# Kernel tuning notes

Measured on AMD Instinct MI355X. Metric: run time of the kernel, lower is better.

Reference implementation:

```python
import jax, jax.numpy as jnp
import numpy as np

B, L, W, H = 4, 4096, 2048, 8
BW = W // H  # block width


def setup_inputs() -> dict:
    key = jax.random.key(0)
    k = jax.random.split(key, 5)
    std = 1.0 / np.sqrt(BW)  # w_init_variance_scale=1.0
    # a_param init: uniform ring in [0.9,0.999] then inverse-softplus
    u = jax.random.uniform(k[4], (W,), minval=0.9**2 + 1e-8, maxval=0.999**2 + 1e-8)
    a_param = jnp.log(jnp.exp(-0.5 * jnp.log(u)) - 1.0)
    return {
        "x": jax.random.normal(k[0], (B, L, W), dtype=jnp.float32),
        "segment_pos": jnp.arange(L, dtype=jnp.int32),
        "prev_h": jnp.zeros((B, W), dtype=jnp.float32),
        "ig_w": std * jax.random.normal(k[1], (H, BW, BW), dtype=jnp.float32),
        "ig_b": jnp.zeros((H, BW), dtype=jnp.float32),
        "ag_w": std * jax.random.normal(k[2], (H, BW, BW), dtype=jnp.float32),
        "ag_b": jnp.zeros((H, BW), dtype=jnp.float32),
        "a_param": a_param,
    }


@jax.custom_vjp
def sqrt_bound(x):
    return jnp.sqrt(x)

def _sb_fwd(x):
    return jnp.sqrt(x), x

def _sb_bwd(x, g):
    _MAX_SQRT_GRADIENT = 1000.0
    return (g / jnp.sqrt(jnp.clip(4.0 * x, 1.0 / _MAX_SQRT_GRADIENT**2)),)

sqrt_bound.defvjp(_sb_fwd, _sb_bwd)


def block_diag_linear(x, w, b):
    # x: [b,l,(h*i)] -> [b,l,h,i]; w: [h,i,j]; b: [h,j]
    bsz, l, _ = x.shape
    xr = x.reshape(bsz, l, H, BW)
    y = jnp.einsum("blhi,hij->blhj", xr, w) + b
    return y.reshape(bsz, l, W)


def reference(x, segment_pos, prev_h, ig_w, ig_b, ag_w, ag_b, a_param):
    reset = (segment_pos == 0)[None, :, None]  # [1,l,1] bool
    gate_x = jax.nn.sigmoid(block_diag_linear(x, ig_w, ig_b))
    gate_a = jax.nn.sigmoid(block_diag_linear(x, ag_w, ag_b))
    log_a = -8.0 * gate_a * jax.nn.softplus(a_param)  # [b,l,w]
    a = jnp.exp(log_a)
    a_square = jnp.exp(2.0 * log_a)
    gated_x = x * gate_x
    multiplier = sqrt_bound(1.0 - a_square)
    multiplier = jnp.where(reset, 1.0, multiplier)
    normalized_x = gated_x * multiplier.astype(x.dtype)
    a = a * (~reset)  # zero recurrence weight at document boundaries

    # linear scan h_t = a_t * h_{t-1} + x_t, accumulate in float32
    def step(h, inp):
        a_t, x_t = inp
        h = a_t.astype(jnp.float32) * h + x_t.astype(jnp.float32)
        return h, h.astype(x.dtype)

    a_t = jnp.swapaxes(jnp.broadcast_to(a, x.shape), 0, 1)  # [l,b,w]
    x_t = jnp.swapaxes(normalized_x, 0, 1)  # [l,b,w]
    last_h, y = jax.lax.scan(step, prev_h, (a_t, x_t))
    y = jnp.swapaxes(y, 0, 1)  # [b,l,w]
    return y, last_h
```

## Files before the change

kernel.cpp:

```cpp
#include <hip/hip_runtime.h>
#include <hip/hip_bf16.h>
#include <cmath>

#define Bq   4
#define Lq   4096
#define Wq   2048
#define Hq   8
#define Mq   (Bq*Lq)
#define TCH  64
#define CCH  (Lq/TCH)

typedef __bf16 bf16;
typedef __attribute__((ext_vector_type(8))) __bf16 bf16x8;
typedef __attribute__((ext_vector_type(4))) float  f32x4;

#define WS_WT    0
#define WS_C     (2*8*256*256*2)
#define WS_PH    (4u<<20)
#define WS_AGG   (WS_PH + (size_t)Mq*Wq*4)
#define WS_CARRY (WS_AGG + (size_t)Bq*CCH*Wq*8)

union pkPH { unsigned u; bf16 v[2]; };

__global__ __launch_bounds__(256) void prep2(const float* __restrict__ ig_w,
                                             const float* __restrict__ ag_w,
                                             const float* __restrict__ a_param,
                                             bf16* __restrict__ wt, float* __restrict__ c_arr) {
    __shared__ float t[64*65];
    int bid = blockIdx.x;
    int kt = bid & 3, nt = (bid >> 2) & 3, h = (bid >> 4) & 7, g = bid >> 7;
    const float* src = g ? ag_w : ig_w;
    int rr = threadIdx.x >> 6, cc = threadIdx.x & 63;
#pragma unroll
    for (int p = 0; p < 16; p++) {
        int kl = p*4 + rr;
        t[kl*65 + cc] = src[h*65536 + (kt*64 + kl)*256 + nt*64 + cc];
    }
    if (bid < 8) {
        float ap = a_param[bid*256 + threadIdx.x];
        c_arr[bid*256 + threadIdx.x] = 8.0f * log1pf(__expf(ap));
    }
    __syncthreads();
#pragma unroll
    for (int p = 0; p < 16; p++) {
        int nl = p*4 + rr;
        wt[((size_t)((g*8 + h)*256) + nt*64 + nl)*256 + kt*64 + cc] = (bf16)t[cc*65 + nl];
    }
}

__global__ __launch_bounds__(256) void gates_scan(
    const float* __restrict__ x, const int* __restrict__ segpos,
    const bf16* __restrict__ wt, const float* __restrict__ igb,
    const float* __restrict__ agb, const float* __restrict__ c_arr,
    unsigned* __restrict__ PH, float2* __restrict__ agg)
{
    union SharedU {
        struct { bf16 As[64*72]; bf16 Wxs[64*72]; bf16 Was[64*72]; } st;
        struct { float A_s[64*65]; float G_s[64*65]; } ep;
    };
    __shared__ SharedU sh;
    __shared__ float segA[4*64], segH[4*64];
    __shared__ unsigned char rs[64];

    const int tid = threadIdx.x;
    const int bx  = blockIdx.x, by = blockIdx.y;
    const int b   = bx >> 6,    c  = bx & 63;
    const int m0  = bx * 64;
    const int h   = by >> 2,    nt = by & 3;
    const int n0  = nt * 64;
    const int wofs = h*256 + n0;

    const int lane = tid & 63, wid = tid >> 6;
    const int wm = wid >> 1, wn = wid & 1;
    const int l16 = lane & 15, quad = lane >> 4;

    if (tid < 64) rs[tid] = (segpos[(m0 + tid) & (Lq-1)] == 0) ? 1 : 0;

    f32x4 accx[2][2], acca[2][2];
#pragma unroll
    for (int i = 0; i < 2; i++)
#pragma unroll
        for (int j = 0; j < 2; j++) {
            accx[i][j] = (f32x4){0.f,0.f,0.f,0.f};
            acca[i][j] = (f32x4){0.f,0.f,0.f,0.f};
        }

    const bf16* wtx = wt + ((size_t)((0*Hq + h)*256 + n0))*256;
    const bf16* wta = wt + ((size_t)((1*Hq + h)*256 + n0))*256;

    for (int kk = 0; kk < 256; kk += 64) {
        __syncthreads();
#pragma unroll
        for (int p = 0; p < 2; p++) {
            int lin = p*2048 + tid*8;
            int r = lin >> 6, cc = lin & 63;
            const float* gp = x + (size_t)(m0 + r)*Wq + h*256 + kk + cc;
            float4 f0 = *(const float4*)gp;
            float4 f1 = *(const float4*)(gp + 4);
            bf16x8 v;
            v[0]=(bf16)f0.x; v[1]=(bf16)f0.y; v[2]=(bf16)f0.z; v[3]=(bf16)f0.w;
            v[4]=(bf16)f1.x; v[5]=(bf16)f1.y; v[6]=(bf16)f1.z; v[7]=(bf16)f1.w;
            *(bf16x8*)&sh.st.As[r*72 + cc] = v;
        }
#pragma unroll
        for (int p = 0; p < 2; p++) {
            int lin = p*2048 + tid*8;
            int r = lin >> 6, cc = lin & 63;
            *(bf16x8*)&sh.st.Wxs[r*72 + cc] = *(const bf16x8*)&wtx[(size_t)r*256 + kk + cc];
            *(bf16x8*)&sh.st.Was[r*72 + cc] = *(const bf16x8*)&wta[(size_t)r*256 + kk + cc];
        }
        __syncthreads();
#pragma unroll
        for (int ks = 0; ks < 2; ks++) {
            bf16x8 af[2], bxf[2], baf[2];
#pragma unroll
            for (int i = 0; i < 2; i++) {
                af[i]  = *(bf16x8*)&sh.st.As [(wm*32 + i*16 + l16)*72 + ks*32 + quad*8];
                bxf[i] = *(bf16x8*)&sh.st.Wxs[(wn*32 + i*16 + l16)*72 + ks*32 + quad*8];
                baf[i] = *(bf16x8*)&sh.st.Was[(wn*32 + i*16 + l16)*72 + ks*32 + quad*8];
            }
#pragma unroll
            for (int i = 0; i < 2; i++)
#pragma unroll
                for (int j = 0; j < 2; j++) {
                    accx[i][j] = __builtin_amdgcn_mfma_f32_16x16x32_bf16(af[i], bxf[j], accx[i][j], 0, 0, 0);
                    acca[i][j] = __builtin_amdgcn_mfma_f32_16x16x32_bf16(af[i], baf[j], acca[i][j], 0, 0, 0);
                }
        }
    }
    __syncthreads();

#pragma unroll
    for (int i = 0; i < 2; i++)
#pragma unroll
        for (int j = 0; j < 2; j++) {
            int col = wn*32 + j*16 + l16;
            int wf  = wofs + col;
            float bxv = igb[wf], bav = agb[wf], cc2 = c_arr[wf];
#pragma unroll
            for (int r = 0; r < 4; r++) {
                int row = wm*32 + i*16 + quad*4 + r;
                float zx = accx[i][j][r] + bxv;
                float za = acca[i][j][r] + bav;
                float gx = __builtin_amdgcn_rcpf(1.f + __expf(-zx));
                float ga = __builtin_amdgcn_rcpf(1.f + __expf(-za));
                float la = -ga * cc2;
                float a  = __expf(la);
                float mult = __builtin_amdgcn_sqrtf(fmaf(-a, a, 1.f));
                if (rs[row]) { a = 0.f; mult = 1.f; }
                sh.ep.A_s[row*65 + col] = a;
                sh.ep.G_s[row*65 + col] = gx * mult;
            }
        }
    __syncthreads();

    const int col2 = tid & 63, seg = tid >> 6;
    float Pl[16], hl[16];
    {
        float A = 1.f, hv = 0.f;
        const float* xp = x + (size_t)(m0 + seg*16)*Wq + wofs + col2;
#pragma unroll
        for (int r = 0; r < 16; r++) {
            int row = seg*16 + r;
            float a  = sh.ep.A_s[row*65 + col2];
            float xn = sh.ep.G_s[row*65 + col2] * xp[(size_t)r*Wq];
            hv = fmaf(a, hv, xn);
            A *= a;
            Pl[r] = A; hl[r] = hv;
        }
        segA[seg*64 + col2] = A;
        segH[seg*64 + col2] = hv;
    }
    __syncthreads();
    float Ap = 1.f, Hp = 0.f;
#pragma unroll
    for (int s = 0; s < 3; s++)
        if (s < seg) {
            Hp = fmaf(segA[s*64 + col2], Hp, segH[s*64 + col2]);
            Ap *= segA[s*64 + col2];
        }

    unsigned* php = PH + (size_t)(m0 + seg*16)*Wq + wofs + col2;
#pragma unroll
    for (int r = 0; r < 16; r++) {
        float Pf = Ap * Pl[r];
        float Hf = fmaf(Pl[r], Hp, hl[r]);
        pkPH pk; pk.v[0] = (bf16)Pf; pk.v[1] = (bf16)Hf;
        php[(size_t)r*Wq] = pk.u;
    }

    if (seg == 3) {
        float Ach = Ap * Pl[15];
        float Hch = fmaf(Pl[15], Hp, hl[15]);
        agg[(size_t)(b*CCH + c)*Wq + wofs + col2] = make_float2(Ach, Hch);
    }
}

__global__ __launch_bounds__(256) void chain_scan(
    const float2* __restrict__ agg, const float* __restrict__ prev_h,
    float* __restrict__ carry, float* __restrict__ last_h)
{
    int tid = blockIdx.x*256 + threadIdx.x;
    int w = tid & (Wq - 1), b = tid >> 11;
    float h = prev_h[tid];
    for (int c = 0; c < CCH; c++) {
        int idx = (b*CCH + c)*Wq + w;
        carry[idx] = h;
        float2 ah = agg[idx];
        h = fmaf(ah.x, h, ah.y);
    }
    last_h[tid] = h;
}

__global__ __launch_bounds__(256) void apply_carry(
    const unsigned* __restrict__ PH, const float* __restrict__ carry,
    float* __restrict__ y)
{
    size_t i4 = ((size_t)blockIdx.x*256 + threadIdx.x) * 4;
    uint4 p = *(const uint4*)(PH + i4);
    int w = (int)(i4 & (Wq - 1));
    int m = (int)(i4 >> 11);
    int b = m >> 12;
    int c = (m & (Lq - 1)) >> 6;
    float4 cr4 = *(const float4*)(carry + (size_t)(b*CCH + c)*Wq + w);
    float4 o;
    pkPH k;
    k.u = p.x; o.x = fmaf((float)k.v[0], cr4.x, (float)k.v[1]);
    k.u = p.y; o.y = fmaf((float)k.v[0], cr4.y, (float)k.v[1]);
    k.u = p.z; o.z = fmaf((float)k.v[0], cr4.z, (float)k.v[1]);
    k.u = p.w; o.w = fmaf((float)k.v[0], cr4.w, (float)k.v[1]);
    *(float4*)(y + i4) = o;
}

extern "C" void kernel_launch(void* const* d_in, const int* in_sizes, int n_in,
                              void* d_out, int out_size, void* d_ws, size_t ws_size,
                              hipStream_t stream) {
    const float* x       = (const float*)d_in[0];
    const int*   segpos  = (const int*)  d_in[1];
    const float* prev_h  = (const float*)d_in[2];
    const float* ig_w    = (const float*)d_in[3];
    const float* ig_b    = (const float*)d_in[4];
    const float* ag_w    = (const float*)d_in[5];
    const float* ag_b    = (const float*)d_in[6];
    const float* a_param = (const float*)d_in[7];
    float* out = (float*)d_out;

    char* ws = (char*)d_ws;
    bf16*   wt    = (bf16*)  (ws + WS_WT);
    float*  c_arr = (float*) (ws + WS_C);
    unsigned* PH  = (unsigned*)(ws + WS_PH);
    float2* agg   = (float2*)(ws + WS_AGG);
    float*  carry = (float*) (ws + WS_CARRY);

    prep2<<<256, 256, 0, stream>>>(ig_w, ag_w, a_param, wt, c_arr);

    dim3 g1(Mq/64, Hq*4);
    gates_scan<<<g1, 256, 0, stream>>>(x, segpos, wt, ig_b, ag_b, c_arr, PH, agg);

    chain_scan<<<(Bq*Wq)/256, 256, 0, stream>>>(agg, prev_h, carry, out + (size_t)Mq*Wq);

    apply_carry<<<(int)(((size_t)Mq*Wq/4)/256), 256, 0, stream>>>(PH, carry, out);
}
```

Measured before the change: 439.3 us.

## Fuse gate GEMM, chunk scan and carry propagation into one persistent sequential kernel

```diff
diff --git a/kernel.cpp b/kernel.cpp
--- a/kernel.cpp
+++ b/kernel.cpp
@@ -7,8 +7,8 @@
 #define Wq   2048
 #define Hq   8
 #define Mq   (Bq*Lq)
-#define TCH  64
-#define CCH  (Lq/TCH)
+#define RCH  64
+#define NCH  (Lq/RCH)
 
 typedef __bf16 bf16;
 typedef __attribute__((ext_vector_type(8))) __bf16 bf16x8;
@@ -16,11 +16,6 @@
 
 #define WS_WT    0
 #define WS_C     (2*8*256*256*2)
-#define WS_PH    (4u<<20)
-#define WS_AGG   (WS_PH + (size_t)Mq*Wq*4)
-#define WS_CARRY (WS_AGG + (size_t)Bq*CCH*Wq*8)
-
-union pkPH { unsigned u; bf16 v[2]; };
 
 __global__ __launch_bounds__(256) void prep2(const float* __restrict__ ig_w,
                                              const float* __restrict__ ag_w,
@@ -48,188 +43,131 @@
     }
 }
 
-__global__ __launch_bounds__(256) void gates_scan(
+__global__ __launch_bounds__(256, 1) void rglru_fused(
     const float* __restrict__ x, const int* __restrict__ segpos,
+    const float* __restrict__ prev_h,
     const bf16* __restrict__ wt, const float* __restrict__ igb,
     const float* __restrict__ agb, const float* __restrict__ c_arr,
-    unsigned* __restrict__ PH, float2* __restrict__ agg)
+    float* __restrict__ out)
 {
-    union SharedU {
-        struct { bf16 As[64*72]; bf16 Wxs[64*72]; bf16 Was[64*72]; } st;
-        struct { float A_s[64*65]; float G_s[64*65]; } ep;
-    };
-    __shared__ SharedU sh;
-    __shared__ float segA[4*64], segH[4*64];
-    __shared__ unsigned char rs[64];
+    __shared__ float A_s[2][RCH*33];
+    __shared__ float G_s[2][RCH*33];
+    __shared__ float X_s[2][RCH*36];
+    __shared__ float sgA[2][256], sgH[2][256];
+    __shared__ float hc[2][32];
 
     const int tid = threadIdx.x;
-    const int bx  = blockIdx.x, by = blockIdx.y;
-    const int b   = bx >> 6,    c  = bx & 63;
-    const int m0  = bx * 64;
-    const int h   = by >> 2,    nt = by & 3;
-    const int n0  = nt * 64;
-    const int wofs = h*256 + n0;
+    const int bid = blockIdx.x;
+    const int h = bid & 7, b = (bid >> 3) & 3, s = bid >> 5;
+    const int lane = tid & 63, wv = tid >> 6;
+    const int l16 = lane & 15, quad = lane >> 4;
+    const int wcol0 = h*256 + s*32;
 
-    const int lane = tid & 63, wid = tid >> 6;
-    const int wm = wid >> 1, wn = wid & 1;
-    const int l16 = lane & 15, quad = lane >> 4;
+    bf16x8 wfx[2][8], wfa[2][8];
+#pragma unroll
+    for (int ct = 0; ct < 2; ct++) {
+        const bf16* px = wt + ((size_t)(h*256 + s*32 + ct*16 + l16))*256 + quad*8;
+        const bf16* pa = px + (size_t)Hq*256*256;
+#pragma unroll
+        for (int ks = 0; ks < 8; ks++) {
+            wfx[ct][ks] = *(const bf16x8*)(px + (size_t)ks*32);
+            wfa[ct][ks] = *(const bf16x8*)(pa + (size_t)ks*32);
+        }
+    }
+    float bxv[2], bav[2], ccv[2];
+#pragma unroll
+    for (int ct = 0; ct < 2; ct++) {
+        int wf = wcol0 + ct*16 + l16;
+        bxv[ct] = igb[wf]; bav[ct] = agb[wf]; ccv[ct] = c_arr[wf];
+    }
+    if (tid < 32) hc[0][tid] = prev_h[b*Wq + wcol0 + tid];
 
-    if (tid < 64) rs[tid] = (segpos[(m0 + tid) & (Lq-1)] == 0) ? 1 : 0;
+    const float* xrow = x + ((size_t)b*Lq + wv*16 + l16)*Wq + h*256 + quad*8;
 
-    f32x4 accx[2][2], acca[2][2];
+    float4 xs[16];
 #pragma unroll
-    for (int i = 0; i < 2; i++)
-#pragma unroll
-        for (int j = 0; j < 2; j++) {
-            accx[i][j] = (f32x4){0.f,0.f,0.f,0.f};
-            acca[i][j] = (f32x4){0.f,0.f,0.f,0.f};
-        }
-
-    const bf16* wtx = wt + ((size_t)((0*Hq + h)*256 + n0))*256;
-    const bf16* wta = wt + ((size_t)((1*Hq + h)*256 + n0))*256;
-
-    for (int kk = 0; kk < 256; kk += 64) {
-        __syncthreads();
-#pragma unroll
-        for (int p = 0; p < 2; p++) {
-            int lin = p*2048 + tid*8;
-            int r = lin >> 6, cc = lin & 63;
-            const float* gp = x + (size_t)(m0 + r)*Wq + h*256 + kk + cc;
-            float4 f0 = *(const float4*)gp;
-            float4 f1 = *(const float4*)(gp + 4);
-            bf16x8 v;
-            v[0]=(bf16)f0.x; v[1]=(bf16)f0.y; v[2]=(bf16)f0.z; v[3]=(bf16)f0.w;
-            v[4]=(bf16)f1.x; v[5]=(bf16)f1.y; v[6]=(bf16)f1.z; v[7]=(bf16)f1.w;
-            *(bf16x8*)&sh.st.As[r*72 + cc] = v;
-        }
-#pragma unroll
-        for (int p = 0; p < 2; p++) {
-            int lin = p*2048 + tid*8;
-            int r = lin >> 6, cc = lin & 63;
-            *(bf16x8*)&sh.st.Wxs[r*72 + cc] = *(const bf16x8*)&wtx[(size_t)r*256 + kk + cc];
-            *(bf16x8*)&sh.st.Was[r*72 + cc] = *(const bf16x8*)&wta[(size_t)r*256 + kk + cc];
-        }
-        __syncthreads();
-#pragma unroll
-        for (int ks = 0; ks < 2; ks++) {
-            bf16x8 af[2], bxf[2], baf[2];
-#pragma unroll
-            for (int i = 0; i < 2; i++) {
-                af[i]  = *(bf16x8*)&sh.st.As [(wm*32 + i*16 + l16)*72 + ks*32 + quad*8];
-                bxf[i] = *(bf16x8*)&sh.st.Wxs[(wn*32 + i*16 + l16)*72 + ks*32 + quad*8];
-                baf[i] = *(bf16x8*)&sh.st.Was[(wn*32 + i*16 + l16)*72 + ks*32 + quad*8];
-            }
-#pragma unroll
-            for (int i = 0; i < 2; i++)
-#pragma unroll
-                for (int j = 0; j < 2; j++) {
-                    accx[i][j] = __builtin_amdgcn_mfma_f32_16x16x32_bf16(af[i], bxf[j], accx[i][j], 0, 0, 0);
-                    acca[i][j] = __builtin_amdgcn_mfma_f32_16x16x32_bf16(af[i], baf[j], acca[i][j], 0, 0, 0);
-                }
-        }
+    for (int ks = 0; ks < 8; ks++) {
+        xs[2*ks]   = *(const float4*)(xrow + ks*32);
+        xs[2*ks+1] = *(const float4*)(xrow + ks*32 + 4);
     }
     __syncthreads();
 
+    int cur = 0;
+    for (int c = 0; c < NCH; ++c) {
+        f32x4 ax[2] = {{0.f,0.f,0.f,0.f},{0.f,0.f,0.f,0.f}};
+        f32x4 aa[2] = {{0.f,0.f,0.f,0.f},{0.f,0.f,0.f,0.f}};
 #pragma unroll
-    for (int i = 0; i < 2; i++)
+        for (int ks = 0; ks < 8; ks++) {
+            float4 u0 = xs[2*ks], u1 = xs[2*ks+1];
+            if (ks == s) {
+                float* xp = &X_s[cur][(wv*16 + l16)*36 + quad*8];
+                *(float4*)xp = u0; *(float4*)(xp + 4) = u1;
+            }
+            bf16x8 af;
+            af[0]=(bf16)u0.x; af[1]=(bf16)u0.y; af[2]=(bf16)u0.z; af[3]=(bf16)u0.w;
+            af[4]=(bf16)u1.x; af[5]=(bf16)u1.y; af[6]=(bf16)u1.z; af[7]=(bf16)u1.w;
+            ax[0] = __builtin_amdgcn_mfma_f32_16x16x32_bf16(af, wfx[0][ks], ax[0], 0,0,0);
+            ax[1] = __builtin_amdgcn_mfma_f32_16x16x32_bf16(af, wfx[1][ks], ax[1], 0,0,0);
+            aa[0] = __builtin_amdgcn_mfma_f32_16x16x32_bf16(af, wfa[0][ks], aa[0], 0,0,0);
+            aa[1] = __builtin_amdgcn_mfma_f32_16x16x32_bf16(af, wfa[1][ks], aa[1], 0,0,0);
+        }
+
+        {
+            const float* xn_ = xrow + (size_t)((c < NCH-1) ? c+1 : c)*RCH*Wq;
 #pragma unroll
-        for (int j = 0; j < 2; j++) {
-            int col = wn*32 + j*16 + l16;
-            int wf  = wofs + col;
-            float bxv = igb[wf], bav = agb[wf], cc2 = c_arr[wf];
+            for (int ks = 0; ks < 8; ks++) {
+                xs[2*ks]   = *(const float4*)(xn_ + ks*32);
+                xs[2*ks+1] = *(const float4*)(xn_ + ks*32 + 4);
+            }
+        }
+
 #pragma unroll
-            for (int r = 0; r < 4; r++) {
-                int row = wm*32 + i*16 + quad*4 + r;
-                float zx = accx[i][j][r] + bxv;
-                float za = acca[i][j][r] + bav;
+        for (int r = 0; r < 4; r++) {
+            int grow = wv*16 + quad*4 + r;
+            bool rst = (segpos[c*RCH + grow] == 0);
+#pragma unroll
+            for (int ct = 0; ct < 2; ct++) {
+                float zx = ax[ct][r] + bxv[ct];
+                float za = aa[ct][r] + bav[ct];
                 float gx = __builtin_amdgcn_rcpf(1.f + __expf(-zx));
                 float ga = __builtin_amdgcn_rcpf(1.f + __expf(-za));
-                float la = -ga * cc2;
-                float a  = __expf(la);
-                float mult = __builtin_amdgcn_sqrtf(fmaf(-a, a, 1.f));
-                if (rs[row]) { a = 0.f; mult = 1.f; }
-                sh.ep.A_s[row*65 + col] = a;
-                sh.ep.G_s[row*65 + col] = gx * mult;
+                float av = __expf(-ga * ccv[ct]);
+                float mult = __builtin_amdgcn_sqrtf(fmaf(-av, av, 1.f));
+                if (rst) { av = 0.f; mult = 1.f; }
+                A_s[cur][grow*33 + ct*16 + l16] = av;
+                G_s[cur][grow*33 + ct*16 + l16] = gx * mult;
             }
         }
-    __syncthreads();
+        __syncthreads();
 
-    const int col2 = tid & 63, seg = tid >> 6;
-    float Pl[16], hl[16];
-    {
+        const int col2 = tid & 31, seg = tid >> 5;
+        float Pl[8], hl[8];
         float A = 1.f, hv = 0.f;
-        const float* xp = x + (size_t)(m0 + seg*16)*Wq + wofs + col2;
 #pragma unroll
-        for (int r = 0; r < 16; r++) {
-            int row = seg*16 + r;
-            float a  = sh.ep.A_s[row*65 + col2];
-            float xn = sh.ep.G_s[row*65 + col2] * xp[(size_t)r*Wq];
-            hv = fmaf(a, hv, xn);
-            A *= a;
+        for (int r = 0; r < 8; r++) {
+            int grow = seg*8 + r;
+            float a  = A_s[cur][grow*33 + col2];
+            float xn = G_s[cur][grow*33 + col2] * X_s[cur][grow*36 + col2];
+            hv = fmaf(a, hv, xn); A *= a;
             Pl[r] = A; hl[r] = hv;
         }
-        segA[seg*64 + col2] = A;
-        segH[seg*64 + col2] = hv;
+        sgA[cur][tid] = A; sgH[cur][tid] = hv;
+        __syncthreads();
+        float h0 = hc[c & 1][col2];
+#pragma unroll
+        for (int sp = 0; sp < 7; sp++)
+            if (sp < seg) h0 = fmaf(sgA[cur][sp*32 + col2], h0, sgH[cur][sp*32 + col2]);
+
+        float* yp = out + ((size_t)b*Lq + c*RCH + seg*8)*Wq + wcol0 + col2;
+#pragma unroll
+        for (int r = 0; r < 8; r++)
+            yp[(size_t)r*Wq] = fmaf(Pl[r], h0, hl[r]);
+
+        if (seg == 7) hc[(c+1) & 1][col2] = fmaf(Pl[7], h0, hl[7]);
+        cur ^= 1;
     }
     __syncthreads();
-    float Ap = 1.f, Hp = 0.f;
-#pragma unroll
-    for (int s = 0; s < 3; s++)
-        if (s < seg) {
-            Hp = fmaf(segA[s*64 + col2], Hp, segH[s*64 + col2]);
-            Ap *= segA[s*64 + col2];
-        }
-
-    unsigned* php = PH + (size_t)(m0 + seg*16)*Wq + wofs + col2;
-#pragma unroll
-    for (int r = 0; r < 16; r++) {
-        float Pf = Ap * Pl[r];
-        float Hf = fmaf(Pl[r], Hp, hl[r]);
-        pkPH pk; pk.v[0] = (bf16)Pf; pk.v[1] = (bf16)Hf;
-        php[(size_t)r*Wq] = pk.u;
-    }
-
-    if (seg == 3) {
-        float Ach = Ap * Pl[15];
-        float Hch = fmaf(Pl[15], Hp, hl[15]);
-        agg[(size_t)(b*CCH + c)*Wq + wofs + col2] = make_float2(Ach, Hch);
-    }
-}
-
-__global__ __launch_bounds__(256) void chain_scan(
-    const float2* __restrict__ agg, const float* __restrict__ prev_h,
-    float* __restrict__ carry, float* __restrict__ last_h)
-{
-    int tid = blockIdx.x*256 + threadIdx.x;
-    int w = tid & (Wq - 1), b = tid >> 11;
-    float h = prev_h[tid];
-    for (int c = 0; c < CCH; c++) {
-        int idx = (b*CCH + c)*Wq + w;
-        carry[idx] = h;
-        float2 ah = agg[idx];
-        h = fmaf(ah.x, h, ah.y);
-    }
-    last_h[tid] = h;
-}
-
-__global__ __launch_bounds__(256) void apply_carry(
-    const unsigned* __restrict__ PH, const float* __restrict__ carry,
-    float* __restrict__ y)
-{
-    size_t i4 = ((size_t)blockIdx.x*256 + threadIdx.x) * 4;
-    uint4 p = *(const uint4*)(PH + i4);
-    int w = (int)(i4 & (Wq - 1));
-    int m = (int)(i4 >> 11);
-    int b = m >> 12;
-    int c = (m & (Lq - 1)) >> 6;
-    float4 cr4 = *(const float4*)(carry + (size_t)(b*CCH + c)*Wq + w);
-    float4 o;
-    pkPH k;
-    k.u = p.x; o.x = fmaf((float)k.v[0], cr4.x, (float)k.v[1]);
-    k.u = p.y; o.y = fmaf((float)k.v[0], cr4.y, (float)k.v[1]);
-    k.u = p.z; o.z = fmaf((float)k.v[0], cr4.z, (float)k.v[1]);
-    k.u = p.w; o.w = fmaf((float)k.v[0], cr4.w, (float)k.v[1]);
-    *(float4*)(y + i4) = o;
+    if (tid < 32) out[(size_t)Mq*Wq + b*Wq + wcol0 + tid] = hc[0][tid];
 }
 
 extern "C" void kernel_launch(void* const* d_in, const int* in_sizes, int n_in,
@@ -248,16 +186,7 @@
     char* ws = (char*)d_ws;
     bf16*   wt    = (bf16*)  (ws + WS_WT);
     float*  c_arr = (float*) (ws + WS_C);
-    unsigned* PH  = (unsigned*)(ws + WS_PH);
-    float2* agg   = (float2*)(ws + WS_AGG);
-    float*  carry = (float*) (ws + WS_CARRY);
 
     prep2<<<256, 256, 0, stream>>>(ig_w, ag_w, a_param, wt, c_arr);
-
-    dim3 g1(Mq/64, Hq*4);
-    gates_scan<<<g1, 256, 0, stream>>>(x, segpos, wt, ig_b, ag_b, c_arr, PH, agg);
-
-    chain_scan<<<(Bq*Wq)/256, 256, 0, stream>>>(agg, prev_h, carry, out + (size_t)Mq*Wq);
-
-    apply_carry<<<(int)(((size_t)Mq*Wq/4)/256), 256, 0, stream>>>(PH, carry, out);
+    rglru_fused<<<256, 256, 0, stream>>>(x, segpos, prev_h, wt, ig_b, ag_b, c_arr, out);
 }
```

Measured after the change: 374.8 us. -14.7%, faster.
